# Optimization experiments

Hardware: AMD Instinct MI355X
Metric: run time of the kernel (lower is better)

The kernel has to match this reference:

```python
import jax, jax.numpy as jnp
import numpy as np
import math

H = 1024          # hidden_size
NUM_LAYERS = 2
V = 32000         # target vocabulary
S = 4096          # source length
W = 64            # window_size
WIN = 2 * W + 1   # max window width (static)
H2 = math.ceil(H / 2)
STD_SQ = (W / 2) ** 2
NEG = -1e30


def setup_inputs() -> dict:
    key = jax.random.key(0)
    ks = jax.random.split(key, 16)
    s = 0.02
    return {
        "source_sentence_length": S,
        "encoder_output": jax.random.normal(ks[0], (S, 1, H), jnp.float32),
        "word": jax.random.randint(ks[1], (1, 1), 0, V),
        "h0": jnp.zeros((NUM_LAYERS, 1, H), jnp.float32),
        "c0": jnp.zeros((NUM_LAYERS, 1, H), jnp.float32),
        "embedding": jax.random.normal(ks[2], (V, H), jnp.float32) * s,
        "lstm_w_ih": jax.random.normal(ks[3], (NUM_LAYERS, 4 * H, H), jnp.float32) * s,
        "lstm_w_hh": jax.random.normal(ks[4], (NUM_LAYERS, 4 * H, H), jnp.float32) * s,
        "lstm_b_ih": jax.random.normal(ks[5], (NUM_LAYERS, 4 * H), jnp.float32) * s,
        "lstm_b_hh": jax.random.normal(ks[6], (NUM_LAYERS, 4 * H), jnp.float32) * s,
        "att_fc1_w": jax.random.normal(ks[7], (H2, H), jnp.float32) * s,
        "att_fc1_b": jax.random.normal(ks[8], (H2,), jnp.float32) * s,
        "att_fc2_w": jax.random.normal(ks[9], (1, H2), jnp.float32) * s,
        "att_fc2_b": jax.random.normal(ks[10], (1,), jnp.float32) * s,
        "fc1_w": jax.random.normal(ks[11], (H, 2 * H), jnp.float32) * s,
        "fc1_b": jax.random.normal(ks[12], (H,), jnp.float32) * s,
        "fc2_w": jax.random.normal(ks[13], (V, H), jnp.float32) * s,
        "fc2_b": jax.random.normal(ks[14], (V,), jnp.float32) * s,
    }


def reference(source_sentence_length, encoder_output, word, h0, c0, embedding,
              lstm_w_ih, lstm_w_hh, lstm_b_ih, lstm_b_hh,
              att_fc1_w, att_fc1_b, att_fc2_w, att_fc2_b,
              fc1_w, fc1_b, fc2_w, fc2_b):
    Sf = jnp.float32(source_sentence_length)
    # embedding lookup (seq=1, batch=1) -> (H,)
    x = embedding[word[0, 0]]
    # stacked LSTM, single time step, torch gate order i,f,g,o
    h_list, c_list = [], []
    for l in range(NUM_LAYERS):
        gates = x @ lstm_w_ih[l].T + lstm_b_ih[l] + h0[l, 0] @ lstm_w_hh[l].T + lstm_b_hh[l]
        i, f, g, o = jnp.split(gates, 4)
        c_new = jax.nn.sigmoid(f) * c0[l, 0] + jax.nn.sigmoid(i) * jnp.tanh(g)
        h_new = jax.nn.sigmoid(o) * jnp.tanh(c_new)
        h_list.append(h_new); c_list.append(c_new)
        x = h_new
    h_n = jnp.stack(h_list)[:, None, :]  # (L,1,H)
    c_n = jnp.stack(c_list)[:, None, :]
    h_t = x  # (H,) decoder output at this step
    # ---- dynamic Gaussian-windowed attention ----
    p = Sf * jax.nn.sigmoid(jnp.tanh(h_t @ att_fc1_w.T + att_fc1_b) @ att_fc2_w.T + att_fc2_b)
    p = p.reshape(())
    ws = jnp.round(jnp.clip(p - W, 0, None)).astype(jnp.int32)                      # clamp(min=0)
    we = jnp.round(jnp.clip(p + W, None, source_sentence_length - 1)).astype(jnp.int32)  # clamp(max=S-1)
    idx = ws + jnp.arange(WIN, dtype=jnp.int32)          # fixed-width window
    valid = idx <= we                                    # replicates [ws:we+1] slice
    h_s = encoder_output[jnp.clip(idx, 0, source_sentence_length - 1), 0, :]
    scores = jnp.where(valid, h_s @ h_t, NEG)
    a = jax.nn.softmax(scores)                           # softmax over window
    gauss = jnp.exp((idx.astype(jnp.float32) - p) / (2.0 * STD_SQ))
    a = jnp.where(valid, a * gauss, 0.0)
    ctx = a @ h_s                                        # (H,)
    # ---- output MLP ----
    out = jnp.tanh(jnp.concatenate([ctx, h_t]) @ fc1_w.T + fc1_b)
    y = jax.nn.log_softmax(out @ fc2_w.T + fc2_b)
    return (y.reshape(1, 1, V), out.reshape(1, 1, H), h_n, c_n, a.reshape(1, 1, WIN))
```

## Files before the change

kernel.cpp:

```cpp
#include <hip/hip_runtime.h>

#define HDIM 1024
#define H4   4096
#define NH2  512
#define VD   32000
#define WINN 129
#define NEGV (-1e30f)

#define X_    0
#define HP_   1024
#define CP_   3072
#define G_    5120
#define ATT1_ 9216
#define CAT_  9728
#define A_    11776
#define SC_   11908
#define IW_   11912
#define LOG_  12288

#define O_Y   0
#define O_OUT 32000
#define O_HN  33024
#define O_CN  35072
#define O_A   37120

__device__ __forceinline__ float dot16f(const float* __restrict__ w, const float* __restrict__ x){
  float4 a0 = *(const float4*)w;
  float4 a1 = *(const float4*)(w+4);
  float4 a2 = *(const float4*)(w+8);
  float4 a3 = *(const float4*)(w+12);
  float acc = 0.f;
  acc += a0.x*x[0] + a0.y*x[1] + a0.z*x[2] + a0.w*x[3];
  acc += a1.x*x[4] + a1.y*x[5] + a1.z*x[6] + a1.w*x[7];
  acc += a2.x*x[8] + a2.y*x[9] + a2.z*x[10] + a2.w*x[11];
  acc += a3.x*x[12] + a3.y*x[13] + a3.z*x[14] + a3.w*x[15];
  return acc;
}
__device__ __forceinline__ float wred(float v){
  #pragma unroll
  for(int off=32; off; off>>=1) v += __shfl_xor(v, off, 64);
  return v;
}
__device__ __forceinline__ float wmax(float v){
  #pragma unroll
  for(int off=32; off; off>>=1) v = fmaxf(v, __shfl_xor(v, off, 64));
  return v;
}
__device__ __forceinline__ float sigf(float x){ return 1.f/(1.f+expf(-x)); }


__global__ __launch_bounds__(256) void k_embed(const int* __restrict__ word,
    const float* __restrict__ emb, const float* __restrict__ h0, const float* __restrict__ c0,
    float* __restrict__ ws){
  int i = blockIdx.x*256 + threadIdx.x;
  if (i < 1024)      ws[X_  + i]        = emb[(size_t)word[0]*HDIM + i];
  else if (i < 3072) ws[HP_ + (i-1024)] = h0[i-1024];
  else               ws[CP_ + (i-3072)] = c0[i-3072];
}

__global__ __launch_bounds__(256) void k_lstm_gemv(
    const float* __restrict__ wih, const float* __restrict__ whh,
    const float* __restrict__ bih, const float* __restrict__ bhh,
    float* __restrict__ ws, int l){
  int gid = blockIdx.x*256 + threadIdx.x;
  int r = gid >> 6, lane = gid & 63;
  const float* wi = wih + ((size_t)r<<10) + lane*16;
  const float* wh = whh + ((size_t)r<<10) + lane*16;
  float acc = dot16f(wi, ws + X_ + lane*16)
            + dot16f(wh, ws + HP_ + l*HDIM + lane*16);
  acc = wred(acc);
  if (lane==0) ws[G_ + r] = acc + bih[r] + bhh[r];
}

__global__ __launch_bounds__(256) void k_lstm_act(float* __restrict__ ws,
    float* __restrict__ hn, float* __restrict__ cn, int l){
  int j = blockIdx.x*256 + threadIdx.x;
  float gi = ws[G_ + j], gf = ws[G_ + 1024 + j], gg = ws[G_ + 2048 + j], go = ws[G_ + 3072 + j];
  float cp = ws[CP_ + l*HDIM + j];
  float c  = sigf(gf)*cp + sigf(gi)*tanhf(gg);
  float h  = sigf(go)*tanhf(c);
  ws[X_ + j] = h;
  if (l==1) ws[CAT_ + HDIM + j] = h;
  hn[l*HDIM + j] = h;
  cn[l*HDIM + j] = c;
}

__global__ __launch_bounds__(256) void k_att1(const float* __restrict__ w,
    const float* __restrict__ b, float* __restrict__ ws){
  int gid = blockIdx.x*256 + threadIdx.x;
  int r = gid >> 6, lane = gid & 63;
  float acc = dot16f(w + ((size_t)r<<10) + lane*16, ws + X_ + lane*16);
  acc = wred(acc);
  if (lane==0) ws[ATT1_ + r] = tanhf(acc + b[r]);
}

__global__ void k_att2(const float* __restrict__ w, const float* __restrict__ b,
    const int* __restrict__ slen, float* __restrict__ ws){
  int lane = threadIdx.x & 63;
  float4 u0 = *(const float4*)(w + lane*8);
  float4 u1 = *(const float4*)(w + lane*8 + 4);
  const float* x = ws + ATT1_ + lane*8;
  float acc = u0.x*x[0] + u0.y*x[1] + u0.z*x[2] + u0.w*x[3]
            + u1.x*x[4] + u1.y*x[5] + u1.z*x[6] + u1.w*x[7];
  acc = wred(acc);
  if (lane==0){
    float val = acc + b[0];
    float Sf  = (float)slen[0];
    float p   = Sf * sigf(val);
    ws[SC_] = p;
    int wsi = (int)rintf(fmaxf(p - 64.f, 0.f));
    int wei = (int)rintf(fminf(p + 64.f, Sf - 1.f));
    ((int*)ws)[IW_]   = wsi;
    ((int*)ws)[IW_+1] = wei;
  }
}

__global__ __launch_bounds__(256) void k_scores(const float* __restrict__ enc,
    const int* __restrict__ slen, float* __restrict__ ws){
  int gid = blockIdx.x*256 + threadIdx.x;
  int k = gid >> 6, lane = gid & 63;
  if (k >= WINN) return;
  int wsi = ((int*)ws)[IW_], wei = ((int*)ws)[IW_+1];
  int idx = wsi + k;
  int smax = slen[0]-1;
  int ci = idx > smax ? smax : (idx < 0 ? 0 : idx);
  float d = dot16f(enc + ((size_t)ci<<10) + lane*16, ws + X_ + lane*16);
  d = wred(d);
  if (lane==0) ws[A_ + k] = (idx <= wei) ? d : NEGV;
}

__global__ void k_softmax(float* __restrict__ ws, float* __restrict__ aout){
  __shared__ float red[8];
  int t = threadIdx.x;
  float p = ws[SC_];
  int wsi = ((int*)ws)[IW_], wei = ((int*)ws)[IW_+1];
  float s = (t < WINN) ? ws[A_ + t] : -INFINITY;
  float m = wmax(s);
  if ((t&63)==0) red[t>>6] = m;
  __syncthreads();
  m = fmaxf(fmaxf(red[0],red[1]), fmaxf(red[2],red[3]));
  float e = (t < WINN) ? expf(s - m) : 0.f;
  float sm = wred(e);
  if ((t&63)==0) red[4 + (t>>6)] = sm;
  __syncthreads();
  sm = red[4]+red[5]+red[6]+red[7];
  if (t < WINN){
    int idx = wsi + t;
    float a = e / sm;
    a = (idx <= wei) ? a * expf(((float)idx - p) * (1.f/2048.f)) : 0.f;
    ws[A_ + t] = a;
    aout[t] = a;
  }
}

__global__ __launch_bounds__(256) void k_ctx(const float* __restrict__ enc,
    const int* __restrict__ slen, float* __restrict__ ws){
  __shared__ float av[WINN];
  __shared__ int   ci[WINN];
  int t = threadIdx.x;
  if (t < WINN){
    av[t] = ws[A_ + t];
    int idx = ((int*)ws)[IW_] + t;
    int smax = slen[0]-1;
    ci[t] = idx > smax ? smax : (idx < 0 ? 0 : idx);
  }
  __syncthreads();
  int i = blockIdx.x*256 + t;
  float acc = 0.f;
  for (int k=0; k<WINN; k++) acc += av[k] * enc[((size_t)ci[k]<<10) + i];
  ws[CAT_ + i] = acc;
}

__global__ __launch_bounds__(256) void k_fc1(const float* __restrict__ w,
    const float* __restrict__ b, float* __restrict__ ws, float* __restrict__ oout){
  int gid = blockIdx.x*256 + threadIdx.x;
  int r = gid >> 6, lane = gid & 63;
  const float* wr = w + ((size_t)r<<11) + lane*32;
  float acc = dot16f(wr, ws + CAT_ + lane*32) + dot16f(wr+16, ws + CAT_ + lane*32 + 16);
  acc = wred(acc);
  if (lane==0){
    float o = tanhf(acc + b[r]);
    ws[X_ + r] = o;
    oout[r] = o;
  }
}

__global__ __launch_bounds__(256) void k_fc2(const float* __restrict__ w,
    const float* __restrict__ b, float* __restrict__ ws){
  int gid = blockIdx.x*256 + threadIdx.x;
  int r = gid >> 6, lane = gid & 63;
  float acc = dot16f(w + ((size_t)r<<10) + lane*16, ws + X_ + lane*16);
  acc = wred(acc);
  if (lane==0) ws[LOG_ + r] = acc + b[r];
}

__global__ __launch_bounds__(1024) void k_lse(float* __restrict__ ws){
  __shared__ float red[16];
  int t = threadIdx.x;
  float m = -INFINITY;
  for (int v=t; v<VD; v+=1024) m = fmaxf(m, ws[LOG_ + v]);
  m = wmax(m);
  if ((t&63)==0) red[t>>6] = m;
  __syncthreads();
  if (t==0){ float mm=red[0]; for(int i=1;i<16;i++) mm=fmaxf(mm,red[i]); red[0]=mm; }
  __syncthreads();
  float M = red[0];
  __syncthreads();
  float s = 0.f;
  for (int v=t; v<VD; v+=1024) s += expf(ws[LOG_ + v] - M);
  s = wred(s);
  if ((t&63)==0) red[t>>6] = s;
  __syncthreads();
  if (t==0){
    float ss=0.f; for(int i=0;i<16;i++) ss+=red[i];
    ws[SC_+1] = M; ws[SC_+2] = logf(ss);
  }
}

__global__ __launch_bounds__(256) void k_y(const float* __restrict__ ws, float* __restrict__ y){
  int v = blockIdx.x*256 + threadIdx.x;
  if (v < VD) y[v] = ws[LOG_ + v] - ws[SC_+1] - ws[SC_+2];
}

extern "C" void kernel_launch(void* const* d_in, const int* in_sizes, int n_in,
                              void* d_out, int out_size, void* d_ws, size_t ws_size,
                              hipStream_t stream) {
  const int*   slen = (const int*)d_in[0];
  const float* enc  = (const float*)d_in[1];
  const int*   word = (const int*)d_in[2];
  const float* h0   = (const float*)d_in[3];
  const float* c0   = (const float*)d_in[4];
  const float* emb  = (const float*)d_in[5];
  const float* wih  = (const float*)d_in[6];
  const float* whh  = (const float*)d_in[7];
  const float* bih  = (const float*)d_in[8];
  const float* bhh  = (const float*)d_in[9];
  const float* a1w  = (const float*)d_in[10];
  const float* a1b  = (const float*)d_in[11];
  const float* a2w  = (const float*)d_in[12];
  const float* a2b  = (const float*)d_in[13];
  const float* f1w  = (const float*)d_in[14];
  const float* f1b  = (const float*)d_in[15];
  const float* f2w  = (const float*)d_in[16];
  const float* f2b  = (const float*)d_in[17];
  float* ws  = (float*)d_ws;
  float* out = (float*)d_out;

  k_embed<<<20,256,0,stream>>>(word, emb, h0, c0, ws);
  for (int l=0; l<2; l++){
    k_lstm_gemv<<<1024,256,0,stream>>>(wih + (size_t)l*H4*HDIM, whh + (size_t)l*H4*HDIM,
                                       bih + l*H4, bhh + l*H4, ws, l);
    k_lstm_act<<<4,256,0,stream>>>(ws, out + O_HN, out + O_CN, l);
  }
  k_att1<<<128,256,0,stream>>>(a1w, a1b, ws);
  k_att2<<<1,64,0,stream>>>(a2w, a2b, slen, ws);
  k_scores<<<33,256,0,stream>>>(enc, slen, ws);
  k_softmax<<<1,256,0,stream>>>(ws, out + O_A);
  k_ctx<<<4,256,0,stream>>>(enc, slen, ws);
  k_fc1<<<256,256,0,stream>>>(f1w, f1b, ws, out + O_OUT);
  k_fc2<<<8000,256,0,stream>>>(f2w, f2b, ws);
  k_lse<<<1,1024,0,stream>>>(ws);
  k_y<<<125,256,0,stream>>>(ws, out + O_Y);
}
```

Baseline: 377.5 us.

## Fuse small kernels, coalesce GEMV loads, and parallelize log-softmax reduction

Removes the embed copy kernel by reading the embedding row and h0/c0 directly in the LSTM kernels. Folds att2 into the scores kernel, where each block recomputes p redundantly. Merges softmax and context into one 1024-thread block. Changes the GEMV lane mapping to strided float4 loads for coalescing, and replaces the single-block LSE with a 32-block partial reduction combined in the output kernel. The cost is fewer launches and less serial work, at the price of redundant recomputation and a single-block context pass.

```diff
diff --git a/kernel.cpp b/kernel.cpp
--- a/kernel.cpp
+++ b/kernel.cpp
@@ -2,20 +2,18 @@
 
 #define HDIM 1024
 #define H4   4096
-#define NH2  512
 #define VD   32000
 #define WINN 129
 #define NEGV (-1e30f)
 
 #define X_    0
-#define HP_   1024
-#define CP_   3072
 #define G_    5120
 #define ATT1_ 9216
 #define CAT_  9728
 #define A_    11776
 #define SC_   11908
 #define IW_   11912
+#define PART_ 12000
 #define LOG_  12288
 
 #define O_Y   0
@@ -24,18 +22,6 @@
 #define O_CN  35072
 #define O_A   37120
 
-__device__ __forceinline__ float dot16f(const float* __restrict__ w, const float* __restrict__ x){
-  float4 a0 = *(const float4*)w;
-  float4 a1 = *(const float4*)(w+4);
-  float4 a2 = *(const float4*)(w+8);
-  float4 a3 = *(const float4*)(w+12);
-  float acc = 0.f;
-  acc += a0.x*x[0] + a0.y*x[1] + a0.z*x[2] + a0.w*x[3];
-  acc += a1.x*x[4] + a1.y*x[5] + a1.z*x[6] + a1.w*x[7];
-  acc += a2.x*x[8] + a2.y*x[9] + a2.z*x[10] + a2.w*x[11];
-  acc += a3.x*x[12] + a3.y*x[13] + a3.z*x[14] + a3.w*x[15];
-  return acc;
-}
 __device__ __forceinline__ float wred(float v){
   #pragma unroll
   for(int off=32; off; off>>=1) v += __shfl_xor(v, off, 64);
@@ -47,136 +33,154 @@
   return v;
 }
 __device__ __forceinline__ float sigf(float x){ return 1.f/(1.f+expf(-x)); }
-
-
-__global__ __launch_bounds__(256) void k_embed(const int* __restrict__ word,
-    const float* __restrict__ emb, const float* __restrict__ h0, const float* __restrict__ c0,
-    float* __restrict__ ws){
-  int i = blockIdx.x*256 + threadIdx.x;
-  if (i < 1024)      ws[X_  + i]        = emb[(size_t)word[0]*HDIM + i];
-  else if (i < 3072) ws[HP_ + (i-1024)] = h0[i-1024];
-  else               ws[CP_ + (i-3072)] = c0[i-3072];
-}
+__device__ __forceinline__ float dot4(float4 a, float4 b){
+  return a.x*b.x + a.y*b.y + a.z*b.z + a.w*b.w;
+}
+
 
 __global__ __launch_bounds__(256) void k_lstm_gemv(
     const float* __restrict__ wih, const float* __restrict__ whh,
     const float* __restrict__ bih, const float* __restrict__ bhh,
-    float* __restrict__ ws, int l){
+    const float* __restrict__ xin, const int* __restrict__ word,
+    const float* __restrict__ emb, const float* __restrict__ hin,
+    float* __restrict__ gout){
   int gid = blockIdx.x*256 + threadIdx.x;
   int r = gid >> 6, lane = gid & 63;
-  const float* wi = wih + ((size_t)r<<10) + lane*16;
-  const float* wh = whh + ((size_t)r<<10) + lane*16;
-  float acc = dot16f(wi, ws + X_ + lane*16)
-            + dot16f(wh, ws + HP_ + l*HDIM + lane*16);
-  acc = wred(acc);
-  if (lane==0) ws[G_ + r] = acc + bih[r] + bhh[r];
-}
-
-__global__ __launch_bounds__(256) void k_lstm_act(float* __restrict__ ws,
-    float* __restrict__ hn, float* __restrict__ cn, int l){
+  const float* xp = word ? (emb + ((size_t)word[0]<<10)) : xin;
+  const float* wi = wih + ((size_t)r<<10);
+  const float* wh = whh + ((size_t)r<<10);
+  float acc = 0.f;
+  #pragma unroll
+  for (int j=0; j<4; j++){
+    int o = lane*4 + 256*j;
+    acc += dot4(*(const float4*)(wi+o), *(const float4*)(xp+o));
+    acc += dot4(*(const float4*)(wh+o), *(const float4*)(hin+o));
+  }
+  acc = wred(acc);
+  if (lane==0) gout[r] = acc + bih[r] + bhh[r];
+}
+
+__global__ __launch_bounds__(256) void k_lstm_act(
+    const float* __restrict__ g, const float* __restrict__ c0l,
+    float* __restrict__ ws, float* __restrict__ hn, float* __restrict__ cn, int last){
   int j = blockIdx.x*256 + threadIdx.x;
-  float gi = ws[G_ + j], gf = ws[G_ + 1024 + j], gg = ws[G_ + 2048 + j], go = ws[G_ + 3072 + j];
-  float cp = ws[CP_ + l*HDIM + j];
-  float c  = sigf(gf)*cp + sigf(gi)*tanhf(gg);
+  float gi = g[j], gf = g[1024+j], gg = g[2048+j], go = g[3072+j];
+  float c  = sigf(gf)*c0l[j] + sigf(gi)*tanhf(gg);
   float h  = sigf(go)*tanhf(c);
   ws[X_ + j] = h;
-  if (l==1) ws[CAT_ + HDIM + j] = h;
-  hn[l*HDIM + j] = h;
-  cn[l*HDIM + j] = c;
+  if (last) ws[CAT_ + HDIM + j] = h;
+  hn[j] = h;
+  cn[j] = c;
 }
 
 __global__ __launch_bounds__(256) void k_att1(const float* __restrict__ w,
     const float* __restrict__ b, float* __restrict__ ws){
   int gid = blockIdx.x*256 + threadIdx.x;
   int r = gid >> 6, lane = gid & 63;
-  float acc = dot16f(w + ((size_t)r<<10) + lane*16, ws + X_ + lane*16);
+  const float* wr = w + ((size_t)r<<10);
+  float acc = 0.f;
+  #pragma unroll
+  for (int j=0; j<4; j++){
+    int o = lane*4 + 256*j;
+    acc += dot4(*(const float4*)(wr+o), *(const float4*)(ws+X_+o));
+  }
   acc = wred(acc);
   if (lane==0) ws[ATT1_ + r] = tanhf(acc + b[r]);
 }
 
-__global__ void k_att2(const float* __restrict__ w, const float* __restrict__ b,
-    const int* __restrict__ slen, float* __restrict__ ws){
-  int lane = threadIdx.x & 63;
-  float4 u0 = *(const float4*)(w + lane*8);
-  float4 u1 = *(const float4*)(w + lane*8 + 4);
-  const float* x = ws + ATT1_ + lane*8;
-  float acc = u0.x*x[0] + u0.y*x[1] + u0.z*x[2] + u0.w*x[3]
-            + u1.x*x[4] + u1.y*x[5] + u1.z*x[6] + u1.w*x[7];
-  acc = wred(acc);
-  if (lane==0){
-    float val = acc + b[0];
-    float Sf  = (float)slen[0];
-    float p   = Sf * sigf(val);
+__global__ __launch_bounds__(256) void k_scores(const float* __restrict__ enc,
+    const int* __restrict__ slen, const float* __restrict__ a2w,
+    const float* __restrict__ a2b, float* __restrict__ ws){
+  int t = threadIdx.x;
+  int lane = t & 63;
+  float pacc = 0.f;
+  #pragma unroll
+  for (int j=0; j<2; j++){
+    int o = lane*4 + 256*j;
+    pacc += dot4(*(const float4*)(a2w+o), *(const float4*)(ws+ATT1_+o));
+  }
+  pacc = wred(pacc);
+  float Sf = (float)slen[0];
+  float p  = Sf * sigf(pacc + a2b[0]);
+  int wsi = (int)rintf(fmaxf(p - 64.f, 0.f));
+  int wei = (int)rintf(fminf(p + 64.f, Sf - 1.f));
+  if (blockIdx.x==0 && t==0){
     ws[SC_] = p;
-    int wsi = (int)rintf(fmaxf(p - 64.f, 0.f));
-    int wei = (int)rintf(fminf(p + 64.f, Sf - 1.f));
     ((int*)ws)[IW_]   = wsi;
     ((int*)ws)[IW_+1] = wei;
   }
-}
-
-__global__ __launch_bounds__(256) void k_scores(const float* __restrict__ enc,
-    const int* __restrict__ slen, float* __restrict__ ws){
-  int gid = blockIdx.x*256 + threadIdx.x;
-  int k = gid >> 6, lane = gid & 63;
+  int k = blockIdx.x*4 + (t>>6);
   if (k >= WINN) return;
-  int wsi = ((int*)ws)[IW_], wei = ((int*)ws)[IW_+1];
   int idx = wsi + k;
   int smax = slen[0]-1;
   int ci = idx > smax ? smax : (idx < 0 ? 0 : idx);
-  float d = dot16f(enc + ((size_t)ci<<10) + lane*16, ws + X_ + lane*16);
-  d = wred(d);
-  if (lane==0) ws[A_ + k] = (idx <= wei) ? d : NEGV;
-}
-
-__global__ void k_softmax(float* __restrict__ ws, float* __restrict__ aout){
-  __shared__ float red[8];
+  const float* er = enc + ((size_t)ci<<10);
+  float acc = 0.f;
+  #pragma unroll
+  for (int j=0; j<4; j++){
+    int o = lane*4 + 256*j;
+    acc += dot4(*(const float4*)(er+o), *(const float4*)(ws+X_+o));
+  }
+  acc = wred(acc);
+  if (lane==0) ws[A_ + k] = (idx <= wei) ? acc : NEGV;
+}
+
+__global__ __launch_bounds__(1024) void k_smctx(const float* __restrict__ enc,
+    const int* __restrict__ slen, float* __restrict__ ws, float* __restrict__ aout){
+  __shared__ float sarr[WINN];
+  __shared__ float av[WINN];
+  __shared__ int   ci[WINN];
+  __shared__ float red[2];
   int t = threadIdx.x;
   float p = ws[SC_];
   int wsi = ((int*)ws)[IW_], wei = ((int*)ws)[IW_+1];
-  float s = (t < WINN) ? ws[A_ + t] : -INFINITY;
-  float m = wmax(s);
-  if ((t&63)==0) red[t>>6] = m;
-  __syncthreads();
-  m = fmaxf(fmaxf(red[0],red[1]), fmaxf(red[2],red[3]));
-  float e = (t < WINN) ? expf(s - m) : 0.f;
-  float sm = wred(e);
-  if ((t&63)==0) red[4 + (t>>6)] = sm;
-  __syncthreads();
-  sm = red[4]+red[5]+red[6]+red[7];
+  int smax = slen[0]-1;
+  if (t < WINN){
+    sarr[t] = ws[A_ + t];
+    int idx = wsi + t;
+    ci[t] = idx > smax ? smax : (idx < 0 ? 0 : idx);
+  }
+  __syncthreads();
+  if (t < 64){
+    float m = fmaxf(sarr[t], sarr[t+64]);
+    if (t==0) m = fmaxf(m, sarr[128]);
+    m = wmax(m);
+    if (t==0) red[0] = m;
+  }
+  __syncthreads();
+  float M = red[0];
+  if (t < 64){
+    float e = expf(sarr[t]-M) + expf(sarr[t+64]-M);
+    if (t==0) e += expf(sarr[128]-M);
+    e = wred(e);
+    if (t==0) red[1] = e;
+  }
+  __syncthreads();
+  float sm = red[1];
   if (t < WINN){
     int idx = wsi + t;
-    float a = e / sm;
+    float a = expf(sarr[t]-M) / sm;
     a = (idx <= wei) ? a * expf(((float)idx - p) * (1.f/2048.f)) : 0.f;
-    ws[A_ + t] = a;
+    av[t] = a;
     aout[t] = a;
   }
-}
-
-__global__ __launch_bounds__(256) void k_ctx(const float* __restrict__ enc,
-    const int* __restrict__ slen, float* __restrict__ ws){
-  __shared__ float av[WINN];
-  __shared__ int   ci[WINN];
-  int t = threadIdx.x;
-  if (t < WINN){
-    av[t] = ws[A_ + t];
-    int idx = ((int*)ws)[IW_] + t;
-    int smax = slen[0]-1;
-    ci[t] = idx > smax ? smax : (idx < 0 ? 0 : idx);
-  }
-  __syncthreads();
-  int i = blockIdx.x*256 + t;
-  float acc = 0.f;
-  for (int k=0; k<WINN; k++) acc += av[k] * enc[((size_t)ci[k]<<10) + i];
-  ws[CAT_ + i] = acc;
+  __syncthreads();
+  float acc = 0.f;
+  for (int k=0; k<WINN; k++) acc += av[k] * enc[((size_t)ci[k]<<10) + t];
+  ws[CAT_ + t] = acc;
 }
 
 __global__ __launch_bounds__(256) void k_fc1(const float* __restrict__ w,
     const float* __restrict__ b, float* __restrict__ ws, float* __restrict__ oout){
   int gid = blockIdx.x*256 + threadIdx.x;
   int r = gid >> 6, lane = gid & 63;
-  const float* wr = w + ((size_t)r<<11) + lane*32;
-  float acc = dot16f(wr, ws + CAT_ + lane*32) + dot16f(wr+16, ws + CAT_ + lane*32 + 16);
+  const float* wr = w + ((size_t)r<<11);
+  float acc = 0.f;
+  #pragma unroll
+  for (int j=0; j<8; j++){
+    int o = lane*4 + 256*j;
+    acc += dot4(*(const float4*)(wr+o), *(const float4*)(ws+CAT_+o));
+  }
   acc = wred(acc);
   if (lane==0){
     float o = tanhf(acc + b[r]);
@@ -185,41 +189,59 @@
   }
 }
 
-__global__ __launch_bounds__(256) void k_fc2(const float* __restrict__ w,
+__global__ __launch_bounds__(512) void k_fc2(const float* __restrict__ w,
     const float* __restrict__ b, float* __restrict__ ws){
-  int gid = blockIdx.x*256 + threadIdx.x;
-  int r = gid >> 6, lane = gid & 63;
-  float acc = dot16f(w + ((size_t)r<<10) + lane*16, ws + X_ + lane*16);
+  int gid = blockIdx.x*512 + threadIdx.x;
+  int r = gid >> 6, lane = gid & 63;
+  const float* wr = w + ((size_t)r<<10);
+  float acc = 0.f;
+  #pragma unroll
+  for (int j=0; j<4; j++){
+    int o = lane*4 + 256*j;
+    acc += dot4(*(const float4*)(wr+o), *(const float4*)(ws+X_+o));
+  }
   acc = wred(acc);
   if (lane==0) ws[LOG_ + r] = acc + b[r];
 }
 
-__global__ __launch_bounds__(1024) void k_lse(float* __restrict__ ws){
-  __shared__ float red[16];
-  int t = threadIdx.x;
-  float m = -INFINITY;
-  for (int v=t; v<VD; v+=1024) m = fmaxf(m, ws[LOG_ + v]);
+__global__ __launch_bounds__(256) void k_lsepart(float* __restrict__ ws){
+  __shared__ float red[4];
+  int b = blockIdx.x, t = threadIdx.x;
+  int base = b*1024;
+  int n = (b==31) ? 256 : 1024;
+  bool act = (t*4 < n);
+  float4 v = make_float4(0.f,0.f,0.f,0.f);
+  if (act) v = *(const float4*)(ws + LOG_ + base + t*4);
+  float m = act ? fmaxf(fmaxf(v.x,v.y), fmaxf(v.z,v.w)) : -INFINITY;
   m = wmax(m);
   if ((t&63)==0) red[t>>6] = m;
   __syncthreads();
-  if (t==0){ float mm=red[0]; for(int i=1;i<16;i++) mm=fmaxf(mm,red[i]); red[0]=mm; }
-  __syncthreads();
-  float M = red[0];
-  __syncthreads();
-  float s = 0.f;
-  for (int v=t; v<VD; v+=1024) s += expf(ws[LOG_ + v] - M);
+  float M = fmaxf(fmaxf(red[0],red[1]), fmaxf(red[2],red[3]));
+  __syncthreads();
+  float s = act ? (expf(v.x-M)+expf(v.y-M)+expf(v.z-M)+expf(v.w-M)) : 0.f;
   s = wred(s);
   if ((t&63)==0) red[t>>6] = s;
   __syncthreads();
   if (t==0){
-    float ss=0.f; for(int i=0;i<16;i++) ss+=red[i];
-    ws[SC_+1] = M; ws[SC_+2] = logf(ss);
+    ws[PART_ + b]      = M;
+    ws[PART_ + 32 + b] = red[0]+red[1]+red[2]+red[3];
   }
 }
 
 __global__ __launch_bounds__(256) void k_y(const float* __restrict__ ws, float* __restrict__ y){
-  int v = blockIdx.x*256 + threadIdx.x;
-  if (v < VD) y[v] = ws[LOG_ + v] - ws[SC_+1] - ws[SC_+2];
+  int i = blockIdx.x*256 + threadIdx.x;
+  float M = -INFINITY;
+  #pragma unroll
+  for (int k=0; k<32; k++) M = fmaxf(M, ws[PART_+k]);
+  float S = 0.f;
+  #pragma unroll
+  for (int k=0; k<32; k++) S += ws[PART_+32+k] * expf(ws[PART_+k] - M);
+  float off = M + logf(S);
+  if (i < 8000){
+    float4 v = *(const float4*)(ws + LOG_ + i*4);
+    v.x -= off; v.y -= off; v.z -= off; v.w -= off;
+    *(float4*)(y + i*4) = v;
+  }
 }
 
 extern "C" void kernel_launch(void* const* d_in, const int* in_sizes, int n_in,
@@ -246,19 +268,19 @@
   float* ws  = (float*)d_ws;
   float* out = (float*)d_out;
 
-  k_embed<<<20,256,0,stream>>>(word, emb, h0, c0, ws);
-  for (int l=0; l<2; l++){
-    k_lstm_gemv<<<1024,256,0,stream>>>(wih + (size_t)l*H4*HDIM, whh + (size_t)l*H4*HDIM,
-                                       bih + l*H4, bhh + l*H4, ws, l);
-    k_lstm_act<<<4,256,0,stream>>>(ws, out + O_HN, out + O_CN, l);
-  }
+  k_lstm_gemv<<<1024,256,0,stream>>>(wih, whh, bih, bhh,
+                                     nullptr, word, emb, h0, ws + G_);
+  k_lstm_act<<<4,256,0,stream>>>(ws + G_, c0, ws, out + O_HN, out + O_CN, 0);
+  k_lstm_gemv<<<1024,256,0,stream>>>(wih + (size_t)H4*HDIM, whh + (size_t)H4*HDIM,
+                                     bih + H4, bhh + H4,
+                                     ws + X_, nullptr, nullptr, h0 + HDIM, ws + G_);
+  k_lstm_act<<<4,256,0,stream>>>(ws + G_, c0 + HDIM, ws, out + O_HN + HDIM, out + O_CN + HDIM, 1);
+
   k_att1<<<128,256,0,stream>>>(a1w, a1b, ws);
-  k_att2<<<1,64,0,stream>>>(a2w, a2b, slen, ws);
-  k_scores<<<33,256,0,stream>>>(enc, slen, ws);
-  k_softmax<<<1,256,0,stream>>>(ws, out + O_A);
-  k_ctx<<<4,256,0,stream>>>(enc, slen, ws);
+  k_scores<<<33,256,0,stream>>>(enc, slen, a2w, a2b, ws);
+  k_smctx<<<1,1024,0,stream>>>(enc, slen, ws, out + O_A);
   k_fc1<<<256,256,0,stream>>>(f1w, f1b, ws, out + O_OUT);
-  k_fc2<<<8000,256,0,stream>>>(f2w, f2b, ws);
-  k_lse<<<1,1024,0,stream>>>(ws);
-  k_y<<<125,256,0,stream>>>(ws, out + O_Y);
-}
+  k_fc2<<<4000,512,0,stream>>>(f2w, f2b, ws);
+  k_lsepart<<<32,256,0,stream>>>(ws);
+  k_y<<<32,256,0,stream>>>(ws, out + O_Y);
+}
```

New measurement: 361.9 us. -4.1%, faster.
